# Kernel optimization log

Measured on AMD Instinct MI355X. Metric: run time of the kernel, lower is better.

The kernel has to match this reference:

```python
import jax, jax.numpy as jnp
import numpy as np

RES = 32            # input grid resolution
OUT_RES = 64        # after subdivide
C = 128             # channels (== out_channels -> skip is identity)
G = 32              # group-norm groups
N = 8192            # active input voxels
EPS = 1e-5

# 8 child offsets for subdivide, 27 stencil offsets for 3x3x3 submanifold conv
_OFFS8 = np.stack(np.meshgrid([0, 1], [0, 1], [0, 1], indexing='ij'), -1).reshape(-1, 3).astype(np.int32)
_OFFS27 = np.stack(np.meshgrid([-1, 0, 1], [-1, 0, 1], [-1, 0, 1], indexing='ij'), -1).reshape(-1, 3).astype(np.int32)


def group_norm(x, gamma, beta, num_groups=G, eps=EPS):
    # sparse group norm over all active voxels of the (single) sample
    n, c = x.shape
    xg = x.reshape(n, num_groups, c // num_groups)
    mean = xg.mean(axis=(0, 2), keepdims=True)
    var = xg.var(axis=(0, 2), keepdims=True)
    xn = (xg - mean) * jax.lax.rsqrt(var + eps)
    return xn.reshape(n, c) * gamma + beta


def subdivide_coords(coords):
    offs = jnp.asarray(_OFFS8)
    return (coords[:, None, :] * 2 + offs[None, :, :]).reshape(-1, 3)  # [8N, 3]


def subm_conv3d(feats, coords, W, b, grid_res):
    # submanifold 3x3x3 sparse conv: outputs only at active sites
    n = feats.shape[0]
    grid = jnp.full((grid_res, grid_res, grid_res), -1, dtype=jnp.int32)
    grid = grid.at[coords[:, 0], coords[:, 1], coords[:, 2]].set(
        jnp.arange(n, dtype=jnp.int32))
    out = jnp.zeros((n, W.shape[-1]), dtype=feats.dtype)
    for k in range(27):  # fixed small stencil loop
        off = jnp.asarray(_OFFS27[k])
        nb = coords + off
        inb = jnp.all((nb >= 0) & (nb < grid_res), axis=1)
        nbc = jnp.clip(nb, 0, grid_res - 1)
        idx = grid[nbc[:, 0], nbc[:, 1], nbc[:, 2]]
        mask = inb & (idx >= 0)
        g = jnp.where(mask[:, None], feats[jnp.where(mask, idx, 0)], 0.0)
        out = out + g @ W[k]
    return out + b


def setup_inputs() -> dict:
    key = jax.random.key(0)
    ks = jax.random.split(key, 8)
    rng = np.random.default_rng(0)
    flat = rng.choice(RES ** 3, size=N, replace=False)
    coords = np.stack([flat // (RES * RES), (flat // RES) % RES, flat % RES],
                      axis=-1).astype(np.int32)
    feats = jax.random.normal(ks[0], (N, C), dtype=jnp.float32)
    gamma1 = 1.0 + 0.1 * jax.random.normal(ks[1], (C,), dtype=jnp.float32)
    beta1 = 0.1 * jax.random.normal(ks[2], (C,), dtype=jnp.float32)
    W1 = jax.random.normal(ks[3], (27, C, C), dtype=jnp.float32) * 0.05
    b1 = jax.random.normal(ks[4], (C,), dtype=jnp.float32) * 0.05
    gamma2 = 1.0 + 0.1 * jax.random.normal(ks[5], (C,), dtype=jnp.float32)
    beta2 = 0.1 * jax.random.normal(ks[6], (C,), dtype=jnp.float32)
    W2 = jax.random.normal(ks[7], (27, C, C), dtype=jnp.float32) * 0.05
    b2 = jax.random.normal(jax.random.fold_in(key, 99), (C,), dtype=jnp.float32) * 0.05
    return {"feats": feats, "gamma1": gamma1, "beta1": beta1, "W1": W1,
            "b1": b1, "gamma2": gamma2, "beta2": beta2, "W2": W2, "b2": b2,
            "coords": jnp.asarray(coords)}


def reference(feats, gamma1, beta1, W1, b1, gamma2, beta2, W2, b2, coords):
    # act_layers: GroupNorm + SiLU at input resolution
    h = jax.nn.silu(group_norm(feats, gamma1, beta1))
    # subdivide both branch and residual (8 children per voxel)
    new_coords = subdivide_coords(coords)          # [8N, 3] in OUT_RES grid
    h = jnp.repeat(h, 8, axis=0)
    x_sub = jnp.repeat(feats, 8, axis=0)
    # out_layers: conv3 -> GN -> SiLU -> conv3 (submanifold, same active set)
    h = subm_conv3d(h, new_coords, W1, b1, OUT_RES)
    h = jax.nn.silu(group_norm(h, gamma2, beta2))
    h = subm_conv3d(h, new_coords, W2, b2, OUT_RES)
    # skip_connection is Identity since out_channels == channels
    return h + x_sub
```

## Files before the change

kernel.cpp:

```cpp
#include <hip/hip_runtime.h>

#define NPAR   8192
#define NCH    65536
#define RES    32
#define EPS    1e-5f

typedef __attribute__((ext_vector_type(8))) short short8;
typedef __attribute__((ext_vector_type(4))) float floatx4;

__device__ __forceinline__ unsigned short f2bf(float f) {
    union { float f; unsigned u; } v; v.f = f;
    unsigned r = v.u + 0x7fffu + ((v.u >> 16) & 1u);
    return (unsigned short)(r >> 16);
}
__device__ __forceinline__ float bf2f(unsigned short b) {
    union { unsigned u; float f; } v; v.u = ((unsigned)b) << 16;
    return v.f;
}
__device__ __forceinline__ void glds16(const void* g, void* l) {
    __builtin_amdgcn_global_load_lds(
        (__attribute__((address_space(1))) const void*)g,
        (__attribute__((address_space(3))) void*)l, 16, 0, 0);
}
__device__ __forceinline__ int k27_of(int o, int s) {
    return (((o >> 2) & 1) + ((s >> 2) & 1)) * 9 +
           (((o >> 1) & 1) + ((s >> 1) & 1)) * 3 +
           ((o & 1) + (s & 1));
}
__device__ __forceinline__ void axis_dlist(int o, int s, int* d, int& n) {
    if (o == 0) { if (s == 0) { d[0] = -1; n = 1; } else { d[0] = 0; d[1] = 1; n = 2; } }
    else        { if (s == 0) { d[0] = -1; d[1] = 0; n = 2; } else { d[0] = 1; n = 1; } }
}

__device__ __forceinline__ void phase_sync() {
    asm volatile("s_waitcnt vmcnt(16)\n\ts_barrier" ::: "memory");
    __builtin_amdgcn_sched_barrier(0);
}

__global__ void k1_kernel(const int* __restrict__ coords, int* __restrict__ grid32,
                          const float* __restrict__ x, float* __restrict__ sum,
                          float* __restrict__ sq) {
    int b = blockIdx.x;
    int t = threadIdx.x;
    if (b < 32) {
        int p = b * 256 + t;
        grid32[(coords[p*3] << 10) + (coords[p*3+1] << 5) + coords[p*3+2]] = p;
    } else {
        __shared__ float s_sum[32], s_sq[32];
        if (t < 32) { s_sum[t] = 0.0f; s_sq[t] = 0.0f; }
        __syncthreads();
        const float4* x4 = (const float4*)x;
        int total = NPAR * 32;
        int idx0 = (b - 32) * 256 + t;
        int g = idx0 & 31;
        float ls = 0.0f, lq = 0.0f;
        for (int idx = idx0; idx < total; idx += 256 * 256) {
            float4 v = x4[idx];
            ls += v.x + v.y + v.z + v.w;
            lq += v.x * v.x + v.y * v.y + v.z * v.z + v.w * v.w;
        }
        atomicAdd(&s_sum[g], ls);
        atomicAdd(&s_sq[g], lq);
        __syncthreads();
        if (t < 32) { atomicAdd(&sum[t], s_sum[t]); atomicAdd(&sq[t], s_sq[t]); }
    }
}

__global__ void k2_kernel(const int* __restrict__ coords, const int* __restrict__ grid32,
                          int* __restrict__ idx_tab, int* __restrict__ pidx27,
                          const float* __restrict__ W1, const float* __restrict__ W2,
                          unsigned short* __restrict__ Wc1f, unsigned short* __restrict__ Wp2,
                          const float* __restrict__ x, const float* __restrict__ sum,
                          const float* __restrict__ sq, const float* __restrict__ gamma,
                          const float* __restrict__ beta, unsigned short* __restrict__ y) {
    int b = blockIdx.x;
    if (b < 32) {
        int p = b * 256 + threadIdx.x;
        int cx = coords[p*3], cy = coords[p*3+1], cz = coords[p*3+2];
        int r27[27];
#pragma unroll
        for (int k = 0; k < 27; ++k) {
            int nx = cx + k / 9 - 1, ny = cy + (k / 3) % 3 - 1, nz = cz + k % 3 - 1;
            int r = -1;
            if ((unsigned)nx < 32u && (unsigned)ny < 32u && (unsigned)nz < 32u) {
                int g = grid32[(nx << 10) + (ny << 5) + nz];
                if ((unsigned)g < (unsigned)NPAR) r = g;
            }
            r27[k] = r;
            pidx27[k * NPAR + p] = r;
        }
#pragma unroll
        for (int k = 0; k < 27; ++k) {
            const int dx = k / 9 - 1, dy = (k / 3) % 3 - 1, dz = k % 3 - 1;
            int v[8];
#pragma unroll
            for (int o = 0; o < 8; ++o) {
                const int ex = ((o >> 2) & 1) + dx;
                const int ey = ((o >> 1) & 1) + dy;
                const int ez = (o & 1) + dz;
                const int ptap = ((ex >> 1) + 1) * 9 + ((ey >> 1) + 1) * 3 + ((ez >> 1) + 1);
                const int slot = ((ex & 1) << 2) + ((ey & 1) << 1) + (ez & 1);
                int r = r27[ptap];
                v[o] = (r >= 0) ? slot * NPAR + r : -1;
            }
            int4* dst = (int4*)&idx_tab[k * NCH + p * 8];
            dst[0] = make_int4(v[0], v[1], v[2], v[3]);
            dst[1] = make_int4(v[4], v[5], v[6], v[7]);
        }
    } else if (b < 248) {
        int rem = (b - 32) * 256 + threadIdx.x;
        int lane = rem & 63;
        int ks   = (rem >> 6) & 3;
        int nb   = (rem >> 8) & 7;
        int tap  = rem >> 11;
        int n  = nb * 16 + (lane & 15);
        int k0 = ks * 32 + (lane >> 4) * 8;
        unsigned short v[8];
#pragma unroll
        for (int j = 0; j < 8; ++j) v[j] = f2bf(W2[tap * 16384 + (k0 + j) * 128 + n]);
        uint4 pk;
        pk.x = (unsigned)v[0] | ((unsigned)v[1] << 16);
        pk.y = (unsigned)v[2] | ((unsigned)v[3] << 16);
        pk.z = (unsigned)v[4] | ((unsigned)v[5] << 16);
        pk.w = (unsigned)v[6] | ((unsigned)v[7] << 16);
        *(uint4*)&Wp2[(long)rem * 8] = pk;
    } else if (b < 760) {
        int rem = (b - 248) * 256 + threadIdx.x;
        int lane  = rem & 63;
        int ks    = (rem >> 6) & 3;
        int nb    = (rem >> 8) & 7;
        int combo = rem >> 11;
        int o = combo >> 3, s = combo & 7;
        int n  = nb * 16 + (lane & 15);
        int k0 = ks * 32 + (lane >> 4) * 8;
        int d0[2], d1[2], d2[2], n0, n1, n2;
        axis_dlist((o >> 2) & 1, (s >> 2) & 1, d0, n0);
        axis_dlist((o >> 1) & 1, (s >> 1) & 1, d1, n1);
        axis_dlist(o & 1,        s & 1,        d2, n2);
        unsigned short v[8];
#pragma unroll
        for (int j = 0; j < 8; ++j) {
            float acc = 0.0f;
            for (int a = 0; a < n0; ++a)
                for (int bb = 0; bb < n1; ++bb)
                    for (int cc = 0; cc < n2; ++cc) {
                        int kk = (d0[a] + 1) * 9 + (d1[bb] + 1) * 3 + (d2[cc] + 1);
                        acc += W1[kk * 16384 + (k0 + j) * 128 + n];
                    }
            v[j] = f2bf(acc);
        }
        uint4 pk;
        pk.x = (unsigned)v[0] | ((unsigned)v[1] << 16);
        pk.y = (unsigned)v[2] | ((unsigned)v[3] << 16);
        pk.z = (unsigned)v[4] | ((unsigned)v[5] << 16);
        pk.w = (unsigned)v[6] | ((unsigned)v[7] << 16);
        *(uint4*)&Wc1f[(long)rem * 8] = pk;
    } else {
        const float4* x4 = (const float4*)x;
        uint2* y2 = (uint2*)y;
        const float4* g4 = (const float4*)gamma;
        const float4* b4 = (const float4*)beta;
        float cnt = (float)NPAR * 4.0f;
        int total = NPAR * 32;
        for (int idx = (b - 760) * 256 + threadIdx.x; idx < total; idx += 256 * 256) {
            int c4 = idx & 31;
            float mean = sum[c4] / cnt;
            float var = sq[c4] / cnt - mean * mean;
            float rstd = rsqrtf(var + EPS);
            float4 v = x4[idx];
            float4 gm = g4[c4];
            float4 bt = b4[c4];
            float a[4] = {v.x, v.y, v.z, v.w};
            float gg[4] = {gm.x, gm.y, gm.z, gm.w};
            float bb[4] = {bt.x, bt.y, bt.z, bt.w};
            unsigned short o[4];
#pragma unroll
            for (int i = 0; i < 4; ++i) {
                float tv = (a[i] - mean) * rstd * gg[i] + bb[i];
                o[i] = f2bf(tv / (1.0f + __expf(-tv)));
            }
            uint2 pk;
            pk.x = (unsigned)o[0] | ((unsigned)o[1] << 16);
            pk.y = (unsigned)o[2] | ((unsigned)o[3] << 16);
            y2[idx] = pk;
        }
    }
}

__global__ void gn_apply_bf16_kernel(unsigned short* __restrict__ x,
                                     const float* __restrict__ sum, const float* __restrict__ sq,
                                     const float* __restrict__ gamma, const float* __restrict__ beta,
                                     int nrows) {
    uint2* x2 = (uint2*)x;
    const float4* g4 = (const float4*)gamma;
    const float4* b4 = (const float4*)beta;
    float cnt = (float)nrows * 4.0f;
    int total = nrows * 32;
    for (int idx = blockIdx.x * blockDim.x + threadIdx.x; idx < total;
         idx += gridDim.x * blockDim.x) {
        int c4 = idx & 31;
        float mean = sum[c4] / cnt;
        float var = sq[c4] / cnt - mean * mean;
        float rstd = rsqrtf(var + EPS);
        uint2 pk = x2[idx];
        float a[4] = {bf2f((unsigned short)(pk.x & 0xffff)), bf2f((unsigned short)(pk.x >> 16)),
                      bf2f((unsigned short)(pk.y & 0xffff)), bf2f((unsigned short)(pk.y >> 16))};
        float4 gm = g4[c4];
        float4 bt = b4[c4];
        float gg[4] = {gm.x, gm.y, gm.z, gm.w};
        float bb[4] = {bt.x, bt.y, bt.z, bt.w};
        unsigned short o[4];
#pragma unroll
        for (int i = 0; i < 4; ++i) {
            float tv = (a[i] - mean) * rstd * gg[i] + bb[i];
            o[i] = f2bf(tv / (1.0f + __expf(-tv)));
        }
        pk.x = (unsigned)o[0] | ((unsigned)o[1] << 16);
        pk.y = (unsigned)o[2] | ((unsigned)o[3] << 16);
        x2[idx] = pk;
    }
}

__device__ __forceinline__ void mfma_phase(
    const unsigned short* __restrict__ Abuf, short8 (&bfr)[4][4],
    floatx4 (&acc)[4][4], int wm, int aswz) {
#pragma unroll
    for (int ks = 0; ks < 4; ++ks) {
        short8 afr[4];
#pragma unroll
        for (int mt = 0; mt < 4; ++mt)
            afr[mt] = *(const short8*)&Abuf[(wm << 13) + (mt << 11) + (ks << 9) + aswz];
#pragma unroll
        for (int mt = 0; mt < 4; ++mt)
#pragma unroll
            for (int nt = 0; nt < 4; ++nt)
                acc[mt][nt] = __builtin_amdgcn_mfma_f32_16x16x32_bf16(
                    afr[mt], bfr[nt][ks], acc[mt][nt], 0, 0, 0);
    }
}
__device__ __forceinline__ void loadB(const unsigned short* __restrict__ Wtap,
                                      short8 (&bfr)[4][4], int wn, int lane) {
#pragma unroll
    for (int nt = 0; nt < 4; ++nt)
#pragma unroll
        for (int ks = 0; ks < 4; ++ks)
            bfr[nt][ks] = *(const short8*)&Wtap[(((wn * 4 + nt) << 2) + ks) * 512 + (lane << 3)];
}
__device__ __forceinline__ void stageA(const unsigned short* __restrict__ Ag,
                                       int iv0, int iv1, const unsigned short* zsrc,
                                       unsigned short* __restrict__ buf,
                                       int base0, int base1, int cchOff) {
    const unsigned short* g0 = (iv0 >= 0) ? Ag + (long)iv0 * 128 : zsrc;
    const unsigned short* g1 = (iv1 >= 0) ? Ag + (long)iv1 * 128 : zsrc;
#pragma unroll
    for (int i = 0; i < 4; ++i) glds16(g0 + i * 32 + cchOff, &buf[base0 + i * 512]);
#pragma unroll
    for (int i = 0; i < 4; ++i) glds16(g1 + i * 32 + cchOff, &buf[base1 + i * 512]);
    __builtin_amdgcn_sched_barrier(0);
}

__global__ void __launch_bounds__(256, 2) conv1_fold_kernel(
    const unsigned short* __restrict__ Ag, const unsigned short* __restrict__ Wc1f,
    const float* __restrict__ bias, const int* __restrict__ pidx27,
    unsigned short* __restrict__ outp, const float* __restrict__ zpage,
    float* __restrict__ gsum, float* __restrict__ gsq) {
    __shared__ unsigned short A_lds[2][16384];

    int t = threadIdx.x;
    int o  = blockIdx.x & 7;
    int P0 = (blockIdx.x >> 3) << 7;
    const unsigned short* Wb = Wc1f + ((long)o << 17);
    int wv = t >> 6, lane = t & 63, quad = lane >> 4, l16 = lane & 15;
    int wm = wv & 1, wn = wv >> 1;
    int r16 = lane >> 2, cch = lane & 3;
    int c0 = wv * 2, c1 = wv * 2 + 1;
    int row0 = ((c0 >> 2) << 6) + ((c0 & 3) << 4) + r16;
    int row1 = ((c1 >> 2) << 6) + ((c1 & 3) << 4) + r16;
    int base0 = ((c0 >> 2) << 13) + ((c0 & 3) << 11);
    int base1 = ((c1 >> 2) << 13) + ((c1 & 3) << 11);
    int cchOff = (cch ^ ((r16 >> 1) & 3)) << 3;
    int aswz = (l16 << 5) + ((quad ^ ((l16 >> 1) & 3)) << 3);
    const unsigned short* zsrc = (const unsigned short*)zpage;

    floatx4 acc[4][4];
#pragma unroll
    for (int mt = 0; mt < 4; ++mt)
#pragma unroll
        for (int nt = 0; nt < 4; ++nt)
            acc[mt][nt] = (floatx4){0.f, 0.f, 0.f, 0.f};
    short8 bA[4][4], bB[4][4];

    stageA(Ag, pidx27[k27_of(o, 0) * NPAR + P0 + row0],
               pidx27[k27_of(o, 0) * NPAR + P0 + row1], zsrc, A_lds[0], base0, base1, cchOff);
    loadB(Wb, bA, wn, lane);
    int nv0 = pidx27[k27_of(o, 1) * NPAR + P0 + row0];
    int nv1 = pidx27[k27_of(o, 1) * NPAR + P0 + row1];
    phase_sync();

#pragma unroll 1
    for (int s = 0; s < 8; s += 2) {
        stageA(Ag, nv0, nv1, zsrc, A_lds[1], base0, base1, cchOff);
        loadB(Wb + ((long)(s + 1) << 14), bB, wn, lane);
        if (s + 2 < 8) {
            nv0 = pidx27[k27_of(o, s + 2) * NPAR + P0 + row0];
            nv1 = pidx27[k27_of(o, s + 2) * NPAR + P0 + row1];
        }
        mfma_phase(A_lds[0], bA, acc, wm, aswz);
        phase_sync();
        if (s + 2 < 8) {
            stageA(Ag, nv0, nv1, zsrc, A_lds[0], base0, base1, cchOff);
            loadB(Wb + ((long)(s + 2) << 14), bA, wn, lane);
            if (s + 3 < 8) {
                nv0 = pidx27[k27_of(o, s + 3) * NPAR + P0 + row0];
                nv1 = pidx27[k27_of(o, s + 3) * NPAR + P0 + row1];
            }
        }
        mfma_phase(A_lds[1], bB, acc, wm, aswz);
        phase_sync();
    }

    float s_[4] = {0.f, 0.f, 0.f, 0.f}, q_[4] = {0.f, 0.f, 0.f, 0.f};
#pragma unroll
    for (int nt = 0; nt < 4; ++nt) {
        int col = wn * 64 + nt * 16 + l16;
        float bv = bias[col];
#pragma unroll
        for (int mt = 0; mt < 4; ++mt) {
#pragma unroll
            for (int r = 0; r < 4; ++r) {
                int prow = wm * 64 + mt * 16 + quad * 4 + r;
                long R = (long)o * NPAR + P0 + prow;
                float v = acc[mt][nt][r] + bv;
                unsigned short u = f2bf(v);
                outp[R * 128 + col] = u;
                float vr = bf2f(u);
                s_[nt] += vr;
                q_[nt] += vr * vr;
            }
        }
    }
    float* sred = (float*)A_lds;
    if (t < 64) sred[t] = 0.0f;
    __syncthreads();
#pragma unroll
    for (int nt = 0; nt < 4; ++nt) {
        int g = (wn * 64 + nt * 16 + l16) >> 2;
        atomicAdd(&sred[g], s_[nt]);
        atomicAdd(&sred[32 + g], q_[nt]);
    }
    __syncthreads();
    if (t < 32) { atomicAdd(&gsum[t], sred[t]); atomicAdd(&gsq[t], sred[32 + t]); }
}

__global__ void __launch_bounds__(256, 2) conv2_kernel(
    const unsigned short* __restrict__ Ag, const unsigned short* __restrict__ Wp,
    const float* __restrict__ bias, const int* __restrict__ idx_tab,
    const float* __restrict__ resid, float* __restrict__ outp,
    const float* __restrict__ zpage) {
    __shared__ unsigned short A_lds[2][16384];

    int t = threadIdx.x;
    int R0 = blockIdx.x * 128;
    int wv = t >> 6, lane = t & 63, quad = lane >> 4, l16 = lane & 15;
    int wm = wv & 1, wn = wv >> 1;
    int r16 = lane >> 2, cch = lane & 3;
    int c0 = wv * 2, c1 = wv * 2 + 1;
    int row0 = ((c0 >> 2) << 6) + ((c0 & 3) << 4) + r16;
    int row1 = ((c1 >> 2) << 6) + ((c1 & 3) << 4) + r16;
    int base0 = ((c0 >> 2) << 13) + ((c0 & 3) << 11);
    int base1 = ((c1 >> 2) << 13) + ((c1 & 3) << 11);
    int cchOff = (cch ^ ((r16 >> 1) & 3)) << 3;
    int aswz = (l16 << 5) + ((quad ^ ((l16 >> 1) & 3)) << 3);
    const unsigned short* zsrc = (const unsigned short*)zpage;

    floatx4 acc[4][4];
#pragma unroll
    for (int mt = 0; mt < 4; ++mt)
#pragma unroll
        for (int nt = 0; nt < 4; ++nt)
            acc[mt][nt] = (floatx4){0.f, 0.f, 0.f, 0.f};
    short8 bA[4][4], bB[4][4];

    stageA(Ag, idx_tab[R0 + row0], idx_tab[R0 + row1], zsrc, A_lds[0], base0, base1, cchOff);
    loadB(Wp, bA, wn, lane);
    int nv0 = idx_tab[NCH + R0 + row0], nv1 = idx_tab[NCH + R0 + row1];
    phase_sync();

#pragma unroll 1
    for (int k = 0; k < 27; k += 2) {
        if (k + 1 < 27) {
            stageA(Ag, nv0, nv1, zsrc, A_lds[1], base0, base1, cchOff);
            loadB(Wp + ((long)(k + 1) << 14), bB, wn, lane);
            if (k + 2 < 27) {
                nv0 = idx_tab[(k + 2) * NCH + R0 + row0];
                nv1 = idx_tab[(k + 2) * NCH + R0 + row1];
            }
        }
        mfma_phase(A_lds[0], bA, acc, wm, aswz);
        phase_sync();
        if (k + 1 < 27) {
            if (k + 2 < 27) {
                stageA(Ag, nv0, nv1, zsrc, A_lds[0], base0, base1, cchOff);
                loadB(Wp + ((long)(k + 2) << 14), bA, wn, lane);
                if (k + 3 < 27) {
                    nv0 = idx_tab[(k + 3) * NCH + R0 + row0];
                    nv1 = idx_tab[(k + 3) * NCH + R0 + row1];
                }
            }
            mfma_phase(A_lds[1], bB, acc, wm, aswz);
            phase_sync();
        }
    }

#pragma unroll
    for (int nt = 0; nt < 4; ++nt) {
        int col = wn * 64 + nt * 16 + l16;
        float bv = bias[col];
#pragma unroll
        for (int mt = 0; mt < 4; ++mt) {
#pragma unroll
            for (int r = 0; r < 4; ++r) {
                int row = wm * 64 + mt * 16 + quad * 4 + r;
                long R = (long)R0 + row;
                float v = acc[mt][nt][r] + bv + resid[(R >> 3) * 128 + col];
                outp[R * 128 + col] = v;
            }
        }
    }
}

extern "C" void kernel_launch(void* const* d_in, const int* in_sizes, int n_in,
                              void* d_out, int out_size, void* d_ws, size_t ws_size,
                              hipStream_t stream) {
    const float* feats  = (const float*)d_in[0];
    const float* gamma1 = (const float*)d_in[1];
    const float* beta1  = (const float*)d_in[2];
    const float* W1     = (const float*)d_in[3];
    const float* b1     = (const float*)d_in[4];
    const float* gamma2 = (const float*)d_in[5];
    const float* beta2  = (const float*)d_in[6];
    const float* W2     = (const float*)d_in[7];
    const float* b2     = (const float*)d_in[8];
    const int*   coords = (const int*)d_in[9];
    float* out = (float*)d_out;

    char* ws = (char*)d_ws;
    unsigned short* h0b  = (unsigned short*)(ws);
    unsigned short* h1b  = (unsigned short*)(ws + (2u << 20));
    unsigned short* Wc1f = (unsigned short*)(ws + (18u << 20));
    unsigned short* Wp2  = (unsigned short*)(ws + (20u << 20));
    int*   grid32        = (int*)  (ws + (21u << 20));
    float* stats         = (float*)(ws + (21u << 20) + 131072);
    float* zpage         = (float*)(ws + (21u << 20) + 131072 + 512);
    int*   idx_tab       = (int*)  (ws + (22u << 20));
    int*   pidx27        = (int*)  (ws + (30u << 20));

    hipMemsetAsync(stats, 0, 1024, stream);

    k1_kernel<<<288, 256, 0, stream>>>(coords, grid32, feats, stats + 0, stats + 32);
    k2_kernel<<<1016, 256, 0, stream>>>(coords, grid32, idx_tab, pidx27,
                                        W1, W2, Wc1f, Wp2,
                                        feats, stats + 0, stats + 32, gamma1, beta1, h0b);

    conv1_fold_kernel<<<8 * (NPAR / 128), 256, 0, stream>>>(h0b, Wc1f, b1, pidx27,
                                                            h1b, zpage,
                                                            stats + 64, stats + 96);

    gn_apply_bf16_kernel<<<1024, 256, 0, stream>>>(h1b, stats + 64, stats + 96, gamma2, beta2, NCH);

    conv2_kernel<<<NCH / 128, 256, 0, stream>>>(h1b, Wp2, b2, idx_tab,
                                                feats, out, zpage);
}
```

Before: 213.9 us.

## Drop per-child index table; derive conv2 neighbors from parent-level pidx27

```diff
diff --git a/kernel.cpp b/kernel.cpp
--- a/kernel.cpp
+++ b/kernel.cpp
@@ -27,14 +27,16 @@
            (((o >> 1) & 1) + ((s >> 1) & 1)) * 3 +
            ((o & 1) + (s & 1));
 }
+__device__ __forceinline__ void tap_ps(int o, int k, int& ptap, int& slotBase) {
+    int ex = ((o >> 2) & 1) + k / 9 - 1;
+    int ey = ((o >> 1) & 1) + (k / 3) % 3 - 1;
+    int ez = (o & 1) + k % 3 - 1;
+    ptap = ((ex >> 1) + 1) * 9 + ((ey >> 1) + 1) * 3 + ((ez >> 1) + 1);
+    slotBase = (((ex & 1) << 2) + ((ey & 1) << 1) + (ez & 1)) * NPAR;
+}
 __device__ __forceinline__ void axis_dlist(int o, int s, int* d, int& n) {
     if (o == 0) { if (s == 0) { d[0] = -1; n = 1; } else { d[0] = 0; d[1] = 1; n = 2; } }
     else        { if (s == 0) { d[0] = -1; d[1] = 0; n = 2; } else { d[0] = 1; n = 1; } }
-}
-
-__device__ __forceinline__ void phase_sync() {
-    asm volatile("s_waitcnt vmcnt(16)\n\ts_barrier" ::: "memory");
-    __builtin_amdgcn_sched_barrier(0);
 }
 
 __global__ void k1_kernel(const int* __restrict__ coords, int* __restrict__ grid32,
@@ -67,7 +69,7 @@
 }
 
 __global__ void k2_kernel(const int* __restrict__ coords, const int* __restrict__ grid32,
-                          int* __restrict__ idx_tab, int* __restrict__ pidx27,
+                          int* __restrict__ pidx27,
                           const float* __restrict__ W1, const float* __restrict__ W2,
                           unsigned short* __restrict__ Wc1f, unsigned short* __restrict__ Wp2,
                           const float* __restrict__ x, const float* __restrict__ sum,
@@ -77,7 +79,6 @@
     if (b < 32) {
         int p = b * 256 + threadIdx.x;
         int cx = coords[p*3], cy = coords[p*3+1], cz = coords[p*3+2];
-        int r27[27];
 #pragma unroll
         for (int k = 0; k < 27; ++k) {
             int nx = cx + k / 9 - 1, ny = cy + (k / 3) % 3 - 1, nz = cz + k % 3 - 1;
@@ -86,26 +87,7 @@
                 int g = grid32[(nx << 10) + (ny << 5) + nz];
                 if ((unsigned)g < (unsigned)NPAR) r = g;
             }
-            r27[k] = r;
             pidx27[k * NPAR + p] = r;
-        }
-#pragma unroll
-        for (int k = 0; k < 27; ++k) {
-            const int dx = k / 9 - 1, dy = (k / 3) % 3 - 1, dz = k % 3 - 1;
-            int v[8];
-#pragma unroll
-            for (int o = 0; o < 8; ++o) {
-                const int ex = ((o >> 2) & 1) + dx;
-                const int ey = ((o >> 1) & 1) + dy;
-                const int ez = (o & 1) + dz;
-                const int ptap = ((ex >> 1) + 1) * 9 + ((ey >> 1) + 1) * 3 + ((ez >> 1) + 1);
-                const int slot = ((ex & 1) << 2) + ((ey & 1) << 1) + (ez & 1);
-                int r = r27[ptap];
-                v[o] = (r >= 0) ? slot * NPAR + r : -1;
-            }
-            int4* dst = (int4*)&idx_tab[k * NCH + p * 8];
-            dst[0] = make_int4(v[0], v[1], v[2], v[3]);
-            dst[1] = make_int4(v[4], v[5], v[6], v[7]);
         }
     } else if (b < 248) {
         int rem = (b - 32) * 256 + threadIdx.x;
@@ -256,7 +238,6 @@
     for (int i = 0; i < 4; ++i) glds16(g0 + i * 32 + cchOff, &buf[base0 + i * 512]);
 #pragma unroll
     for (int i = 0; i < 4; ++i) glds16(g1 + i * 32 + cchOff, &buf[base1 + i * 512]);
-    __builtin_amdgcn_sched_barrier(0);
 }
 
 __global__ void __launch_bounds__(256, 2) conv1_fold_kernel(
@@ -295,7 +276,7 @@
     loadB(Wb, bA, wn, lane);
     int nv0 = pidx27[k27_of(o, 1) * NPAR + P0 + row0];
     int nv1 = pidx27[k27_of(o, 1) * NPAR + P0 + row1];
-    phase_sync();
+    __syncthreads();
 
 #pragma unroll 1
     for (int s = 0; s < 8; s += 2) {
@@ -306,7 +287,7 @@
             nv1 = pidx27[k27_of(o, s + 2) * NPAR + P0 + row1];
         }
         mfma_phase(A_lds[0], bA, acc, wm, aswz);
-        phase_sync();
+        __syncthreads();
         if (s + 2 < 8) {
             stageA(Ag, nv0, nv1, zsrc, A_lds[0], base0, base1, cchOff);
             loadB(Wb + ((long)(s + 2) << 14), bA, wn, lane);
@@ -316,7 +297,7 @@
             }
         }
         mfma_phase(A_lds[1], bB, acc, wm, aswz);
-        phase_sync();
+        __syncthreads();
     }
 
     float s_[4] = {0.f, 0.f, 0.f, 0.f}, q_[4] = {0.f, 0.f, 0.f, 0.f};
@@ -354,13 +335,14 @@
 
 __global__ void __launch_bounds__(256, 2) conv2_kernel(
     const unsigned short* __restrict__ Ag, const unsigned short* __restrict__ Wp,
-    const float* __restrict__ bias, const int* __restrict__ idx_tab,
+    const float* __restrict__ bias, const int* __restrict__ pidx27,
     const float* __restrict__ resid, float* __restrict__ outp,
     const float* __restrict__ zpage) {
     __shared__ unsigned short A_lds[2][16384];
 
     int t = threadIdx.x;
-    int R0 = blockIdx.x * 128;
+    int o  = blockIdx.x & 7;
+    int P0 = (blockIdx.x >> 3) << 7;
     int wv = t >> 6, lane = t & 63, quad = lane >> 4, l16 = lane & 15;
     int wm = wv & 1, wn = wv >> 1;
     int r16 = lane >> 2, cch = lane & 3;
@@ -381,10 +363,23 @@
             acc[mt][nt] = (floatx4){0.f, 0.f, 0.f, 0.f};
     short8 bA[4][4], bB[4][4];
 
-    stageA(Ag, idx_tab[R0 + row0], idx_tab[R0 + row1], zsrc, A_lds[0], base0, base1, cchOff);
+    {
+        int pt, sb; tap_ps(o, 0, pt, sb);
+        int r0 = pidx27[pt * NPAR + P0 + row0];
+        int r1 = pidx27[pt * NPAR + P0 + row1];
+        stageA(Ag, r0 >= 0 ? sb + r0 : -1, r1 >= 0 ? sb + r1 : -1,
+               zsrc, A_lds[0], base0, base1, cchOff);
+    }
     loadB(Wp, bA, wn, lane);
-    int nv0 = idx_tab[NCH + R0 + row0], nv1 = idx_tab[NCH + R0 + row1];
-    phase_sync();
+    int nv0, nv1;
+    {
+        int pt, sb; tap_ps(o, 1, pt, sb);
+        int r0 = pidx27[pt * NPAR + P0 + row0];
+        int r1 = pidx27[pt * NPAR + P0 + row1];
+        nv0 = r0 >= 0 ? sb + r0 : -1;
+        nv1 = r1 >= 0 ? sb + r1 : -1;
+    }
+    __syncthreads();
 
 #pragma unroll 1
     for (int k = 0; k < 27; k += 2) {
@@ -392,23 +387,29 @@
             stageA(Ag, nv0, nv1, zsrc, A_lds[1], base0, base1, cchOff);
             loadB(Wp + ((long)(k + 1) << 14), bB, wn, lane);
             if (k + 2 < 27) {
-                nv0 = idx_tab[(k + 2) * NCH + R0 + row0];
-                nv1 = idx_tab[(k + 2) * NCH + R0 + row1];
+                int pt, sb; tap_ps(o, k + 2, pt, sb);
+                int r0 = pidx27[pt * NPAR + P0 + row0];
+                int r1 = pidx27[pt * NPAR + P0 + row1];
+                nv0 = r0 >= 0 ? sb + r0 : -1;
+                nv1 = r1 >= 0 ? sb + r1 : -1;
             }
         }
         mfma_phase(A_lds[0], bA, acc, wm, aswz);
-        phase_sync();
+        __syncthreads();
         if (k + 1 < 27) {
             if (k + 2 < 27) {
                 stageA(Ag, nv0, nv1, zsrc, A_lds[0], base0, base1, cchOff);
                 loadB(Wp + ((long)(k + 2) << 14), bA, wn, lane);
                 if (k + 3 < 27) {
-                    nv0 = idx_tab[(k + 3) * NCH + R0 + row0];
-                    nv1 = idx_tab[(k + 3) * NCH + R0 + row1];
+                    int pt, sb; tap_ps(o, k + 3, pt, sb);
+                    int r0 = pidx27[pt * NPAR + P0 + row0];
+                    int r1 = pidx27[pt * NPAR + P0 + row1];
+                    nv0 = r0 >= 0 ? sb + r0 : -1;
+                    nv1 = r1 >= 0 ? sb + r1 : -1;
                 }
             }
             mfma_phase(A_lds[1], bB, acc, wm, aswz);
-            phase_sync();
+            __syncthreads();
         }
     }
 
@@ -420,10 +421,10 @@
         for (int mt = 0; mt < 4; ++mt) {
 #pragma unroll
             for (int r = 0; r < 4; ++r) {
-                int row = wm * 64 + mt * 16 + quad * 4 + r;
-                long R = (long)R0 + row;
-                float v = acc[mt][nt][r] + bv + resid[(R >> 3) * 128 + col];
-                outp[R * 128 + col] = v;
+                int prow = wm * 64 + mt * 16 + quad * 4 + r;
+                long p = (long)P0 + prow;
+                float v = acc[mt][nt][r] + bv + resid[p * 128 + col];
+                outp[(p * 8 + o) * 128 + col] = v;
             }
         }
     }
@@ -452,13 +453,12 @@
     int*   grid32        = (int*)  (ws + (21u << 20));
     float* stats         = (float*)(ws + (21u << 20) + 131072);
     float* zpage         = (float*)(ws + (21u << 20) + 131072 + 512);
-    int*   idx_tab       = (int*)  (ws + (22u << 20));
-    int*   pidx27        = (int*)  (ws + (30u << 20));
+    int*   pidx27        = (int*)  (ws + (22u << 20));
 
     hipMemsetAsync(stats, 0, 1024, stream);
 
     k1_kernel<<<288, 256, 0, stream>>>(coords, grid32, feats, stats + 0, stats + 32);
-    k2_kernel<<<1016, 256, 0, stream>>>(coords, grid32, idx_tab, pidx27,
+    k2_kernel<<<1016, 256, 0, stream>>>(coords, grid32, pidx27,
                                         W1, W2, Wc1f, Wp2,
                                         feats, stats + 0, stats + 32, gamma1, beta1, h0b);
 
@@ -468,6 +468,6 @@
 
     gn_apply_bf16_kernel<<<1024, 256, 0, stream>>>(h1b, stats + 64, stats + 96, gamma2, beta2, NCH);
 
-    conv2_kernel<<<NCH / 128, 256, 0, stream>>>(h1b, Wp2, b2, idx_tab,
-                                                feats, out, zpage);
-}
+    conv2_kernel<<<8 * (NPAR / 128), 256, 0, stream>>>(h1b, Wp2, b2, pidx27,
+                                                       feats, out, zpage);
+}
```

After: 216.1 us. About the same (+1.0%).

## Change warp tiling to 1x4 column split and use plain syncthreads

Applied to the files above, without the earlier changes.

```diff
diff --git a/kernel.cpp b/kernel.cpp
--- a/kernel.cpp
+++ b/kernel.cpp
@@ -30,11 +30,6 @@
 __device__ __forceinline__ void axis_dlist(int o, int s, int* d, int& n) {
     if (o == 0) { if (s == 0) { d[0] = -1; n = 1; } else { d[0] = 0; d[1] = 1; n = 2; } }
     else        { if (s == 0) { d[0] = -1; d[1] = 0; n = 2; } else { d[0] = 1; n = 1; } }
-}
-
-__device__ __forceinline__ void phase_sync() {
-    asm volatile("s_waitcnt vmcnt(16)\n\ts_barrier" ::: "memory");
-    __builtin_amdgcn_sched_barrier(0);
 }
 
 __global__ void k1_kernel(const int* __restrict__ coords, int* __restrict__ grid32,
@@ -222,29 +217,29 @@
 }
 
 __device__ __forceinline__ void mfma_phase(
-    const unsigned short* __restrict__ Abuf, short8 (&bfr)[4][4],
-    floatx4 (&acc)[4][4], int wm, int aswz) {
+    const unsigned short* __restrict__ Abuf, short8 (&bfr)[2][4],
+    floatx4 (&acc)[8][2], int aswz) {
 #pragma unroll
     for (int ks = 0; ks < 4; ++ks) {
-        short8 afr[4];
-#pragma unroll
-        for (int mt = 0; mt < 4; ++mt)
-            afr[mt] = *(const short8*)&Abuf[(wm << 13) + (mt << 11) + (ks << 9) + aswz];
-#pragma unroll
-        for (int mt = 0; mt < 4; ++mt)
-#pragma unroll
-            for (int nt = 0; nt < 4; ++nt)
+        short8 afr[8];
+#pragma unroll
+        for (int mt = 0; mt < 8; ++mt)
+            afr[mt] = *(const short8*)&Abuf[(mt << 11) + (ks << 9) + aswz];
+#pragma unroll
+        for (int mt = 0; mt < 8; ++mt)
+#pragma unroll
+            for (int nt = 0; nt < 2; ++nt)
                 acc[mt][nt] = __builtin_amdgcn_mfma_f32_16x16x32_bf16(
                     afr[mt], bfr[nt][ks], acc[mt][nt], 0, 0, 0);
     }
 }
 __device__ __forceinline__ void loadB(const unsigned short* __restrict__ Wtap,
-                                      short8 (&bfr)[4][4], int wn, int lane) {
-#pragma unroll
-    for (int nt = 0; nt < 4; ++nt)
+                                      short8 (&bfr)[2][4], int wn, int lane) {
+#pragma unroll
+    for (int nt = 0; nt < 2; ++nt)
 #pragma unroll
         for (int ks = 0; ks < 4; ++ks)
-            bfr[nt][ks] = *(const short8*)&Wtap[(((wn * 4 + nt) << 2) + ks) * 512 + (lane << 3)];
+            bfr[nt][ks] = *(const short8*)&Wtap[(((wn * 2 + nt) << 2) + ks) * 512 + (lane << 3)];
 }
 __device__ __forceinline__ void stageA(const unsigned short* __restrict__ Ag,
                                        int iv0, int iv1, const unsigned short* zsrc,
@@ -256,7 +251,6 @@
     for (int i = 0; i < 4; ++i) glds16(g0 + i * 32 + cchOff, &buf[base0 + i * 512]);
 #pragma unroll
     for (int i = 0; i < 4; ++i) glds16(g1 + i * 32 + cchOff, &buf[base1 + i * 512]);
-    __builtin_amdgcn_sched_barrier(0);
 }
 
 __global__ void __launch_bounds__(256, 2) conv1_fold_kernel(
@@ -271,7 +265,7 @@
     int P0 = (blockIdx.x >> 3) << 7;
     const unsigned short* Wb = Wc1f + ((long)o << 17);
     int wv = t >> 6, lane = t & 63, quad = lane >> 4, l16 = lane & 15;
-    int wm = wv & 1, wn = wv >> 1;
+    int wn = wv;
     int r16 = lane >> 2, cch = lane & 3;
     int c0 = wv * 2, c1 = wv * 2 + 1;
     int row0 = ((c0 >> 2) << 6) + ((c0 & 3) << 4) + r16;
@@ -282,20 +276,20 @@
     int aswz = (l16 << 5) + ((quad ^ ((l16 >> 1) & 3)) << 3);
     const unsigned short* zsrc = (const unsigned short*)zpage;
 
-    floatx4 acc[4][4];
-#pragma unroll
-    for (int mt = 0; mt < 4; ++mt)
-#pragma unroll
-        for (int nt = 0; nt < 4; ++nt)
+    floatx4 acc[8][2];
+#pragma unroll
+    for (int mt = 0; mt < 8; ++mt)
+#pragma unroll
+        for (int nt = 0; nt < 2; ++nt)
             acc[mt][nt] = (floatx4){0.f, 0.f, 0.f, 0.f};
-    short8 bA[4][4], bB[4][4];
+    short8 bA[2][4], bB[2][4];
 
     stageA(Ag, pidx27[k27_of(o, 0) * NPAR + P0 + row0],
                pidx27[k27_of(o, 0) * NPAR + P0 + row1], zsrc, A_lds[0], base0, base1, cchOff);
     loadB(Wb, bA, wn, lane);
     int nv0 = pidx27[k27_of(o, 1) * NPAR + P0 + row0];
     int nv1 = pidx27[k27_of(o, 1) * NPAR + P0 + row1];
-    phase_sync();
+    __syncthreads();
 
 #pragma unroll 1
     for (int s = 0; s < 8; s += 2) {
@@ -305,8 +299,8 @@
             nv0 = pidx27[k27_of(o, s + 2) * NPAR + P0 + row0];
             nv1 = pidx27[k27_of(o, s + 2) * NPAR + P0 + row1];
         }
-        mfma_phase(A_lds[0], bA, acc, wm, aswz);
-        phase_sync();
+        mfma_phase(A_lds[0], bA, acc, aswz);
+        __syncthreads();
         if (s + 2 < 8) {
             stageA(Ag, nv0, nv1, zsrc, A_lds[0], base0, base1, cchOff);
             loadB(Wb + ((long)(s + 2) << 14), bA, wn, lane);
@@ -315,20 +309,20 @@
                 nv1 = pidx27[k27_of(o, s + 3) * NPAR + P0 + row1];
             }
         }
-        mfma_phase(A_lds[1], bB, acc, wm, aswz);
-        phase_sync();
-    }
-
-    float s_[4] = {0.f, 0.f, 0.f, 0.f}, q_[4] = {0.f, 0.f, 0.f, 0.f};
-#pragma unroll
-    for (int nt = 0; nt < 4; ++nt) {
-        int col = wn * 64 + nt * 16 + l16;
+        mfma_phase(A_lds[1], bB, acc, aswz);
+        __syncthreads();
+    }
+
+    float s_[2] = {0.f, 0.f}, q_[2] = {0.f, 0.f};
+#pragma unroll
+    for (int nt = 0; nt < 2; ++nt) {
+        int col = wn * 32 + nt * 16 + l16;
         float bv = bias[col];
 #pragma unroll
-        for (int mt = 0; mt < 4; ++mt) {
+        for (int mt = 0; mt < 8; ++mt) {
 #pragma unroll
             for (int r = 0; r < 4; ++r) {
-                int prow = wm * 64 + mt * 16 + quad * 4 + r;
+                int prow = mt * 16 + quad * 4 + r;
                 long R = (long)o * NPAR + P0 + prow;
                 float v = acc[mt][nt][r] + bv;
                 unsigned short u = f2bf(v);
@@ -343,8 +337,8 @@
     if (t < 64) sred[t] = 0.0f;
     __syncthreads();
 #pragma unroll
-    for (int nt = 0; nt < 4; ++nt) {
-        int g = (wn * 64 + nt * 16 + l16) >> 2;
+    for (int nt = 0; nt < 2; ++nt) {
+        int g = (wn * 32 + nt * 16 + l16) >> 2;
         atomicAdd(&sred[g], s_[nt]);
         atomicAdd(&sred[32 + g], q_[nt]);
     }
@@ -362,7 +356,7 @@
     int t = threadIdx.x;
     int R0 = blockIdx.x * 128;
     int wv = t >> 6, lane = t & 63, quad = lane >> 4, l16 = lane & 15;
-    int wm = wv & 1, wn = wv >> 1;
+    int wn = wv;
     int r16 = lane >> 2, cch = lane & 3;
     int c0 = wv * 2, c1 = wv * 2 + 1;
     int row0 = ((c0 >> 2) << 6) + ((c0 & 3) << 4) + r16;
@@ -373,18 +367,18 @@
     int aswz = (l16 << 5) + ((quad ^ ((l16 >> 1) & 3)) << 3);
     const unsigned short* zsrc = (const unsigned short*)zpage;
 
-    floatx4 acc[4][4];
-#pragma unroll
-    for (int mt = 0; mt < 4; ++mt)
-#pragma unroll
-        for (int nt = 0; nt < 4; ++nt)
+    floatx4 acc[8][2];
+#pragma unroll
+    for (int mt = 0; mt < 8; ++mt)
+#pragma unroll
+        for (int nt = 0; nt < 2; ++nt)
             acc[mt][nt] = (floatx4){0.f, 0.f, 0.f, 0.f};
-    short8 bA[4][4], bB[4][4];
+    short8 bA[2][4], bB[2][4];
 
     stageA(Ag, idx_tab[R0 + row0], idx_tab[R0 + row1], zsrc, A_lds[0], base0, base1, cchOff);
     loadB(Wp, bA, wn, lane);
     int nv0 = idx_tab[NCH + R0 + row0], nv1 = idx_tab[NCH + R0 + row1];
-    phase_sync();
+    __syncthreads();
 
 #pragma unroll 1
     for (int k = 0; k < 27; k += 2) {
@@ -396,8 +390,8 @@
                 nv1 = idx_tab[(k + 2) * NCH + R0 + row1];
             }
         }
-        mfma_phase(A_lds[0], bA, acc, wm, aswz);
-        phase_sync();
+        mfma_phase(A_lds[0], bA, acc, aswz);
+        __syncthreads();
         if (k + 1 < 27) {
             if (k + 2 < 27) {
                 stageA(Ag, nv0, nv1, zsrc, A_lds[0], base0, base1, cchOff);
@@ -407,20 +401,20 @@
                     nv1 = idx_tab[(k + 3) * NCH + R0 + row1];
                 }
             }
-            mfma_phase(A_lds[1], bB, acc, wm, aswz);
-            phase_sync();
-        }
-    }
-
-#pragma unroll
-    for (int nt = 0; nt < 4; ++nt) {
-        int col = wn * 64 + nt * 16 + l16;
+            mfma_phase(A_lds[1], bB, acc, aswz);
+            __syncthreads();
+        }
+    }
+
+#pragma unroll
+    for (int nt = 0; nt < 2; ++nt) {
+        int col = wn * 32 + nt * 16 + l16;
         float bv = bias[col];
 #pragma unroll
-        for (int mt = 0; mt < 4; ++mt) {
+        for (int mt = 0; mt < 8; ++mt) {
 #pragma unroll
             for (int r = 0; r < 4; ++r) {
-                int row = wm * 64 + mt * 16 + quad * 4 + r;
+                int row = mt * 16 + quad * 4 + r;
                 long R = (long)R0 + row;
                 float v = acc[mt][nt][r] + bv + resid[(R >> 3) * 128 + col];
                 outp[R * 128 + col] = v;
```

After: 201.7 us. -5.7%, faster.
